# Kernel tuning notes

Hardware: AMD Instinct MI355X
Metric: run time of the kernel (lower is better)

Reference implementation:

```python
import jax, jax.numpy as jnp
import numpy as np

N_NODES = 100000
N_EDGES = 3200000
D_IN = 128


def setup_inputs() -> dict:
    key = jax.random.key(0)
    k1, k2, k3, k4 = jax.random.split(key, 4)
    x = jax.random.normal(k1, (N_NODES, D_IN), dtype=jnp.float32)
    edge_index = jax.random.randint(k2, (2, N_EDGES), 0, N_NODES, dtype=jnp.int64)
    W1 = jax.random.normal(k3, (D_IN, 16), dtype=jnp.float32) * (1.0 / np.sqrt(D_IN))
    b1 = jnp.zeros((16,), dtype=jnp.float32)
    W2 = jax.random.normal(k4, (16, 2), dtype=jnp.float32) * (1.0 / np.sqrt(16))
    b2 = jnp.zeros((2,), dtype=jnp.float32)
    return {"x": x, "edge_index": edge_index, "W1": W1, "b1": b1, "W2": W2, "b2": b2}


def _gcn_norm(edge_index, n_nodes):
    # Add self-loops, then symmetric degree normalization (PyG gcn_norm).
    loops = jnp.arange(n_nodes, dtype=edge_index.dtype)
    row = jnp.concatenate([edge_index[0], loops])  # source
    col = jnp.concatenate([edge_index[1], loops])  # target
    ones = jnp.ones(row.shape[0], dtype=jnp.float32)
    deg = jax.ops.segment_sum(ones, col, num_segments=n_nodes)
    dis = jnp.where(deg > 0, jax.lax.rsqrt(deg), 0.0)  # deg^{-1/2}
    norm = dis[row] * dis[col]  # [E+N]
    return row, col, norm


def _gcn_conv(x, row, col, norm, W, b, n_nodes):
    h = x @ W  # transform first (PyG order): [N, out]
    msgs = h[row] * norm[:, None]  # gather from source, scale
    agg = jax.ops.segment_sum(msgs, col, num_segments=n_nodes)  # scatter-add to target
    return agg + b


def reference(x, edge_index, W1, b1, W2, b2):
    n = x.shape[0]
    row, col, norm = _gcn_norm(edge_index, n)
    h = _gcn_conv(x, row, col, norm, W1, b1, n)
    h = jax.nn.relu(h)
    h = _gcn_conv(h, row, col, norm, W2, b2, n)
    return jax.nn.log_softmax(h, axis=1)
```

## Files before the change

kernel.cpp:

```cpp
#include <hip/hip_runtime.h>
#include <hip/hip_fp16.h>

#define DIN 128
#define BSH 7
#define BSIZE 128
#define NBMAX 800
#define CAP 4480
#define CHUNK 8192
#define PB 512

__global__ __launch_bounds__(PB) void place_kernel(const int* __restrict__ row,
                                                   const int* __restrict__ col,
                                                   int* __restrict__ cur,
                                                   int* __restrict__ sp, int E, int NB) {
    __shared__ int pk[CHUNK];
    __shared__ unsigned short bkid[CHUNK];
    __shared__ int lcnt[NBMAX], lstart[NBMAX], gofs[NBMAX], lcur[NBMAX];
    __shared__ int sst[PB];
    int t = threadIdx.x;
    int e0 = blockIdx.x * CHUNK;
    int cnt = min(CHUNK, E - e0);

    for (int i = t; i < NBMAX; i += PB) { lcnt[i] = 0; lcur[i] = 0; }
    __syncthreads();
    for (int i = t; i < cnt; i += PB)
        atomicAdd(&lcnt[col[e0 + i] >> BSH], 1);
    __syncthreads();
    int b2i = t * 2;
    int v0 = (b2i + 0 < NBMAX) ? lcnt[b2i + 0] : 0;
    int v1 = (b2i + 1 < NBMAX) ? lcnt[b2i + 1] : 0;
    int tot = v0 + v1;
    sst[t] = tot;
    __syncthreads();
    for (int d = 1; d < PB; d <<= 1) {
        int tmp = (t >= d) ? sst[t - d] : 0;
        __syncthreads();
        sst[t] += tmp;
        __syncthreads();
    }
    int ex = sst[t] - tot;
    if (b2i + 0 < NBMAX) lstart[b2i + 0] = ex;
    if (b2i + 1 < NBMAX) lstart[b2i + 1] = ex + v0;
    __syncthreads();
    for (int b = t; b < NB; b += PB) {
        int c = lcnt[b];
        int gb = c ? atomicAdd(&cur[b], c) : 0;
        gofs[b] = b * CAP + gb - lstart[b];
    }
    __syncthreads();
    for (int i = t; i < cnt; i += PB) {
        int r  = row[e0 + i];
        int cc = col[e0 + i];
        int b  = cc >> BSH;
        int rk = atomicAdd(&lcur[b], 1);
        int pos = lstart[b] + rk;
        pk[pos]   = ((cc & (BSIZE - 1)) << 17) | r;
        bkid[pos] = (unsigned short)b;
    }
    __syncthreads();
    for (int i = t; i < cnt; i += PB)
        sp[gofs[bkid[i]] + i] = pk[i];
}

__global__ __launch_bounds__(256) void bdeg_kernel(const int* __restrict__ sp,
                                                   const int* __restrict__ cur,
                                                   float* __restrict__ dis, int N) {
    __shared__ int lcnt[BSIZE];
    int b = blockIdx.x;
    int t = threadIdx.x;
    int cntb = cur[b];
    const int* src = sp + (size_t)b * CAP;
    if (t < BSIZE) lcnt[t] = 0;
    __syncthreads();
    int n4 = cntb >> 2;
    const int4* src4 = (const int4*)src;
    for (int i = t; i < n4; i += 256) {
        int4 v = src4[i];
        atomicAdd(&lcnt[v.x >> 17], 1);
        atomicAdd(&lcnt[v.y >> 17], 1);
        atomicAdd(&lcnt[v.z >> 17], 1);
        atomicAdd(&lcnt[v.w >> 17], 1);
    }
    for (int i = (n4 << 2) + t; i < cntb; i += 256)
        atomicAdd(&lcnt[src[i] >> 17], 1);
    __syncthreads();
    if (t < BSIZE) {
        int gt = b * BSIZE + t;
        if (gt < N) dis[gt] = rsqrtf((float)lcnt[t] + 1.0f);
    }
}

__global__ __launch_bounds__(256) void xw1_kernel(const float* __restrict__ x,
                                                  const float* __restrict__ W1,
                                                  const float* __restrict__ dis,
                                                  __half* __restrict__ hp, int N) {
    __shared__ float xs[64 * 132];
    __shared__ float wt[16 * 132];
    int t = threadIdx.x;
    int base = blockIdx.x * 64;
    for (int i = t; i < DIN * 16; i += 256) {
        int d = i >> 4, k = i & 15;
        wt[k * 132 + d] = W1[i];
    }
    int nrow = min(64, N - base);
    for (int i = t; i < 64 * 32; i += 256) {
        int r = i >> 5, c4 = i & 31;
        float4 v = make_float4(0.f, 0.f, 0.f, 0.f);
        if (r < nrow) v = *(const float4*)(x + (size_t)(base + r) * DIN + c4 * 4);
        *(float4*)(xs + r * 132 + c4 * 4) = v;
    }
    __syncthreads();
    int np = t >> 3;
    int kp = t & 7;
    int n0 = np * 2, k0 = kp * 2;
    const float4* xa = (const float4*)(xs + n0 * 132);
    const float4* xb = (const float4*)(xs + (n0 + 1) * 132);
    const float4* wa = (const float4*)(wt + k0 * 132);
    const float4* wb = (const float4*)(wt + (k0 + 1) * 132);
    float a00 = 0.f, a01 = 0.f, a10 = 0.f, a11 = 0.f;
    #pragma unroll 8
    for (int d4 = 0; d4 < 32; d4++) {
        float4 va = xa[d4], vb = xb[d4], u0 = wa[d4], u1 = wb[d4];
        a00 += va.x*u0.x + va.y*u0.y + va.z*u0.z + va.w*u0.w;
        a01 += va.x*u1.x + va.y*u1.y + va.z*u1.z + va.w*u1.w;
        a10 += vb.x*u0.x + vb.y*u0.y + vb.z*u0.z + vb.w*u0.w;
        a11 += vb.x*u1.x + vb.y*u1.y + vb.z*u1.z + vb.w*u1.w;
    }
    int n = base + n0;
    if (n < N) {
        float d = dis[n];
        hp[(size_t)n * 16 + k0 + 0] = __float2half(a00 * d);
        hp[(size_t)n * 16 + k0 + 1] = __float2half(a01 * d);
    }
    n++;
    if (n < N) {
        float d = dis[n];
        hp[(size_t)n * 16 + k0 + 0] = __float2half(a10 * d);
        hp[(size_t)n * 16 + k0 + 1] = __float2half(a11 * d);
    }
}

__global__ __launch_bounds__(256) void bsg1_kernel(int* sp,
                                                   const int* __restrict__ cur,
                                                   const float* __restrict__ dis,
                                                   const __half2* __restrict__ hp2,
                                                   const float* __restrict__ b1,
                                                   const float* __restrict__ W2,
                                                   int* __restrict__ off,
                                                   float* __restrict__ gp, int N) {
    __shared__ int spk[CAP];
    __shared__ int ss[CAP];
    __shared__ int lcnt[BSIZE], lstart[BSIZE], lcur[BSIZE], sc[BSIZE];
    int b = blockIdx.x;
    int t = threadIdx.x;
    int cntb = cur[b];
    int* reg = sp + (size_t)b * CAP;
    if (t < BSIZE) { lcnt[t] = 0; lcur[t] = 0; }
    __syncthreads();
    for (int i = t; i < cntb; i += 256) {
        int v = reg[i];
        spk[i] = v;
        atomicAdd(&lcnt[v >> 17], 1);
    }
    __syncthreads();
    int v = (t < BSIZE) ? lcnt[t] : 0;
    if (t < BSIZE) sc[t] = v;
    __syncthreads();
    for (int d = 1; d < BSIZE; d <<= 1) {
        int tmp = (t < BSIZE && t >= d) ? sc[t - d] : 0;
        __syncthreads();
        if (t < BSIZE) sc[t] += tmp;
        __syncthreads();
    }
    if (t < BSIZE) lstart[t] = sc[t] - v;
    __syncthreads();
    for (int i = t; i < cntb; i += 256) {
        int vv = spk[i];
        int lt = vv >> 17;
        int rk = atomicAdd(&lcur[lt], 1);
        ss[lstart[lt] + rk] = vv & 0x1FFFF;
    }
    __syncthreads();
    for (int i = t; i < cntb; i += 256) reg[i] = ss[i];
    if (t < BSIZE) {
        off[b * (BSIZE + 1) + t] = b * CAP + lstart[t];
    } else if (t == BSIZE) {
        off[b * (BSIZE + 1) + BSIZE] = b * CAP + cntb;
    }
    int k2  = t & 7;
    int ltg = t >> 3;
    #pragma unroll
    for (int r4 = 0; r4 < 4; r4++) {
        int lt = r4 * 32 + ltg;
        int gt = b * BSIZE + lt;
        if (gt < N) {
            int j0 = lstart[lt];
            int j1 = j0 + lcnt[lt];
            float2 acc0 = __half22float2(hp2[(size_t)gt * 8 + k2]);
            float2 acc1 = make_float2(0.f, 0.f);
            float2 acc2 = make_float2(0.f, 0.f);
            float2 acc3 = make_float2(0.f, 0.f);
            int j = j0;
            for (; j + 3 < j1; j += 4) {
                int r0 = ss[j + 0], r1 = ss[j + 1], r2 = ss[j + 2], r3 = ss[j + 3];
                float2 h0 = __half22float2(hp2[(size_t)r0 * 8 + k2]);
                float2 h1 = __half22float2(hp2[(size_t)r1 * 8 + k2]);
                float2 h2 = __half22float2(hp2[(size_t)r2 * 8 + k2]);
                float2 h3 = __half22float2(hp2[(size_t)r3 * 8 + k2]);
                acc0.x += h0.x; acc0.y += h0.y;
                acc1.x += h1.x; acc1.y += h1.y;
                acc2.x += h2.x; acc2.y += h2.y;
                acc3.x += h3.x; acc3.y += h3.y;
            }
            for (; j < j1; j++) {
                int r = ss[j];
                float2 hv = __half22float2(hp2[(size_t)r * 8 + k2]);
                acc0.x += hv.x; acc0.y += hv.y;
            }
            float2 acc = make_float2(acc0.x + acc1.x + acc2.x + acc3.x,
                                     acc0.y + acc1.y + acc2.y + acc3.y);
            float d = dis[gt];
            int k0 = k2 * 2;
            float v0 = fmaxf(fmaf(acc.x, d, b1[k0 + 0]), 0.0f);
            float v1 = fmaxf(fmaf(acc.y, d, b1[k0 + 1]), 0.0f);
            float p0 = v0 * W2[k0 * 2 + 0] + v1 * W2[k0 * 2 + 2];
            float p1 = v0 * W2[k0 * 2 + 1] + v1 * W2[k0 * 2 + 3];
            p0 += __shfl_xor(p0, 1); p1 += __shfl_xor(p1, 1);
            p0 += __shfl_xor(p0, 2); p1 += __shfl_xor(p1, 2);
            p0 += __shfl_xor(p0, 4); p1 += __shfl_xor(p1, 4);
            if (k2 == 0) *(float2*)(gp + (size_t)gt * 2) = make_float2(p0 * d, p1 * d);
        }
    }
}

__global__ __launch_bounds__(256) void g2_kernel(const int* __restrict__ sp,
                                                 const int* __restrict__ off,
                                                 const float* __restrict__ dis,
                                                 const float* __restrict__ gp,
                                                 const float* __restrict__ b2,
                                                 float* __restrict__ out, int N) {
    int t = blockIdx.x * 256 + threadIdx.x;
    int c    = t >> 2;
    int slot = t & 3;
    if (c >= N) return;
    int idx = (c >> BSH) * (BSIZE + 1) + (c & (BSIZE - 1));
    int j0 = off[idx];
    int j1 = off[idx + 1];
    float a0 = 0.0f, a1v = 0.0f;
    for (int j = j0 + slot; j < j1; j += 4) {
        int r = sp[j];
        float2 gv = *(const float2*)(gp + (size_t)r * 2);
        a0  += gv.x;
        a1v += gv.y;
    }
    a0 += __shfl_xor(a0, 1); a1v += __shfl_xor(a1v, 1);
    a0 += __shfl_xor(a0, 2); a1v += __shfl_xor(a1v, 2);
    if (slot == 0) {
        float2 self = *(const float2*)(gp + (size_t)c * 2);
        float d = dis[c];
        float o0 = (a0  + self.x) * d + b2[0];
        float o1 = (a1v + self.y) * d + b2[1];
        float m = fmaxf(o0, o1);
        float lse = m + logf(expf(o0 - m) + expf(o1 - m));
        *(float2*)(out + (size_t)c * 2) = make_float2(o0 - lse, o1 - lse);
    }
}

extern "C" void kernel_launch(void* const* d_in, const int* in_sizes, int n_in,
                              void* d_out, int out_size, void* d_ws, size_t ws_size,
                              hipStream_t stream) {
    const float* x  = (const float*)d_in[0];
    const int*   ei = (const int*)d_in[1];
    const float* W1 = (const float*)d_in[2];
    const float* b1 = (const float*)d_in[3];
    const float* W2 = (const float*)d_in[4];
    const float* b2 = (const float*)d_in[5];
    float* out = (float*)d_out;

    const int N = in_sizes[0] / DIN;
    const int E = in_sizes[1] / 2;
    const int* row = ei;
    const int* col = ei + E;
    const int NB = (N + BSIZE - 1) / BSIZE;

    int*    cur = (int*)d_ws;
    float*  dis = (float*)(cur + NBMAX);
    int*    off = (int*)(dis + N);
    int*    sp  = off + (size_t)NB * (BSIZE + 1);
    __half* hp  = (__half*)(sp + (size_t)NB * CAP);
    float*  gp  = (float*)(hp + (size_t)N * 16);

    hipMemsetAsync(cur, 0, NBMAX * 4, stream);
    place_kernel<<<(E + CHUNK - 1) / CHUNK, PB, 0, stream>>>(row, col, cur, sp, E, NB);
    bdeg_kernel <<<NB, 256, 0, stream>>>(sp, cur, dis, N);
    xw1_kernel  <<<(N + 63) / 64, 256, 0, stream>>>(x, W1, dis, hp, N);
    bsg1_kernel <<<NB, 256, 0, stream>>>(sp, cur, dis, (const __half2*)hp, b1, W2, off, gp, N);
    g2_kernel   <<<(int)(((size_t)N * 4 + 255) / 256), 256, 0, stream>>>(sp, off, dis, gp, b2, out, N);
}
```

Baseline: 203.4 us.

## Fuse degree computation into xw1 and split bucket sort into half-buckets

Removes the separate degree kernel: each xw1 block scans its parent bucket, counts in-degree for its 64 nodes, writes dis, and applies it from shared memory. The sort-and-gather kernel now runs two blocks per 128-node bucket, each sorting only its half into a new srt2 buffer, which halves shared memory per block and doubles the block count. Each block still reads the whole parent bucket, so bucket reads are duplicated. The second-layer gather uses 8 lanes per node instead of 4.

```diff
diff --git a/kernel.cpp b/kernel.cpp
--- a/kernel.cpp
+++ b/kernel.cpp
@@ -4,8 +4,11 @@
 #define DIN 128
 #define BSH 7
 #define BSIZE 128
+#define HB 64
 #define NBMAX 800
+#define NBMAX2 1600
 #define CAP 4480
+#define HCAP 2560
 #define CHUNK 8192
 #define PB 512
 
@@ -62,42 +65,21 @@
         sp[gofs[bkid[i]] + i] = pk[i];
 }
 
-__global__ __launch_bounds__(256) void bdeg_kernel(const int* __restrict__ sp,
-                                                   const int* __restrict__ cur,
-                                                   float* __restrict__ dis, int N) {
-    __shared__ int lcnt[BSIZE];
-    int b = blockIdx.x;
-    int t = threadIdx.x;
-    int cntb = cur[b];
-    const int* src = sp + (size_t)b * CAP;
-    if (t < BSIZE) lcnt[t] = 0;
-    __syncthreads();
-    int n4 = cntb >> 2;
-    const int4* src4 = (const int4*)src;
-    for (int i = t; i < n4; i += 256) {
-        int4 v = src4[i];
-        atomicAdd(&lcnt[v.x >> 17], 1);
-        atomicAdd(&lcnt[v.y >> 17], 1);
-        atomicAdd(&lcnt[v.z >> 17], 1);
-        atomicAdd(&lcnt[v.w >> 17], 1);
-    }
-    for (int i = (n4 << 2) + t; i < cntb; i += 256)
-        atomicAdd(&lcnt[src[i] >> 17], 1);
-    __syncthreads();
-    if (t < BSIZE) {
-        int gt = b * BSIZE + t;
-        if (gt < N) dis[gt] = rsqrtf((float)lcnt[t] + 1.0f);
-    }
-}
-
 __global__ __launch_bounds__(256) void xw1_kernel(const float* __restrict__ x,
                                                   const float* __restrict__ W1,
-                                                  const float* __restrict__ dis,
+                                                  const int* __restrict__ sp,
+                                                  const int* __restrict__ cur,
+                                                  float* __restrict__ dis,
                                                   __half* __restrict__ hp, int N) {
     __shared__ float xs[64 * 132];
     __shared__ float wt[16 * 132];
+    __shared__ int   lcnt[HB];
+    __shared__ float disl[HB];
     int t = threadIdx.x;
-    int base = blockIdx.x * 64;
+    int blk = blockIdx.x;
+    int base = blk * 64;
+    int B = blk >> 1, h = blk & 1;
+    if (t < HB) lcnt[t] = 0;
     for (int i = t; i < DIN * 16; i += 256) {
         int d = i >> 4, k = i & 15;
         wt[k * 132 + d] = W1[i];
@@ -108,6 +90,20 @@
         float4 v = make_float4(0.f, 0.f, 0.f, 0.f);
         if (r < nrow) v = *(const float4*)(x + (size_t)(base + r) * DIN + c4 * 4);
         *(float4*)(xs + r * 132 + c4 * 4) = v;
+    }
+    __syncthreads();
+    int cntb = cur[B];
+    const int* reg = sp + (size_t)B * CAP;
+    for (int i = t; i < cntb; i += 256) {
+        int lc = reg[i] >> 17;
+        if ((lc >> 6) == h) atomicAdd(&lcnt[lc & 63], 1);
+    }
+    __syncthreads();
+    if (t < HB) {
+        float dv = rsqrtf((float)lcnt[t] + 1.0f);
+        disl[t] = dv;
+        int gt = base + t;
+        if (gt < N) dis[gt] = dv;
     }
     __syncthreads();
     int np = t >> 3;
@@ -128,71 +124,75 @@
     }
     int n = base + n0;
     if (n < N) {
-        float d = dis[n];
+        float d = disl[n0];
         hp[(size_t)n * 16 + k0 + 0] = __float2half(a00 * d);
         hp[(size_t)n * 16 + k0 + 1] = __float2half(a01 * d);
     }
     n++;
     if (n < N) {
-        float d = dis[n];
+        float d = disl[n0 + 1];
         hp[(size_t)n * 16 + k0 + 0] = __float2half(a10 * d);
         hp[(size_t)n * 16 + k0 + 1] = __float2half(a11 * d);
     }
 }
 
-__global__ __launch_bounds__(256) void bsg1_kernel(int* sp,
+__global__ __launch_bounds__(256) void bsg1_kernel(const int* __restrict__ sp,
                                                    const int* __restrict__ cur,
                                                    const float* __restrict__ dis,
                                                    const __half2* __restrict__ hp2,
                                                    const float* __restrict__ b1,
                                                    const float* __restrict__ W2,
+                                                   int* __restrict__ srt2,
                                                    int* __restrict__ off,
                                                    float* __restrict__ gp, int N) {
-    __shared__ int spk[CAP];
-    __shared__ int ss[CAP];
-    __shared__ int lcnt[BSIZE], lstart[BSIZE], lcur[BSIZE], sc[BSIZE];
-    int b = blockIdx.x;
+    __shared__ int ss[HCAP];
+    __shared__ int lcnt[HB], lstart[HB], lcur[HB], sc[HB];
+    int b2 = blockIdx.x;
+    int B = b2 >> 1, h = b2 & 1;
     int t = threadIdx.x;
-    int cntb = cur[b];
-    int* reg = sp + (size_t)b * CAP;
-    if (t < BSIZE) { lcnt[t] = 0; lcur[t] = 0; }
+    int cntb = cur[B];
+    const int* reg = sp + (size_t)B * CAP;
+    if (t < HB) { lcnt[t] = 0; lcur[t] = 0; }
     __syncthreads();
     for (int i = t; i < cntb; i += 256) {
-        int v = reg[i];
-        spk[i] = v;
-        atomicAdd(&lcnt[v >> 17], 1);
-    }
-    __syncthreads();
-    int v = (t < BSIZE) ? lcnt[t] : 0;
-    if (t < BSIZE) sc[t] = v;
-    __syncthreads();
-    for (int d = 1; d < BSIZE; d <<= 1) {
-        int tmp = (t < BSIZE && t >= d) ? sc[t - d] : 0;
+        int lc = reg[i] >> 17;
+        if ((lc >> 6) == h) atomicAdd(&lcnt[lc & 63], 1);
+    }
+    __syncthreads();
+    int v = (t < HB) ? lcnt[t] : 0;
+    if (t < HB) sc[t] = v;
+    __syncthreads();
+    for (int d = 1; d < HB; d <<= 1) {
+        int tmp = (t < HB && t >= d) ? sc[t - d] : 0;
         __syncthreads();
-        if (t < BSIZE) sc[t] += tmp;
+        if (t < HB) sc[t] += tmp;
         __syncthreads();
     }
-    if (t < BSIZE) lstart[t] = sc[t] - v;
+    if (t < HB) lstart[t] = sc[t] - v;
     __syncthreads();
     for (int i = t; i < cntb; i += 256) {
-        int vv = spk[i];
-        int lt = vv >> 17;
-        int rk = atomicAdd(&lcur[lt], 1);
-        ss[lstart[lt] + rk] = vv & 0x1FFFF;
-    }
-    __syncthreads();
-    for (int i = t; i < cntb; i += 256) reg[i] = ss[i];
-    if (t < BSIZE) {
-        off[b * (BSIZE + 1) + t] = b * CAP + lstart[t];
-    } else if (t == BSIZE) {
-        off[b * (BSIZE + 1) + BSIZE] = b * CAP + cntb;
+        int vv = reg[i];
+        int lc = vv >> 17;
+        if ((lc >> 6) == h) {
+            int l = lc & 63;
+            int rk = atomicAdd(&lcur[l], 1);
+            ss[lstart[l] + rk] = vv & 0x1FFFF;
+        }
+    }
+    __syncthreads();
+    int hcnt = sc[HB - 1];
+    for (int i = t; i < hcnt; i += 256) srt2[(size_t)b2 * HCAP + i] = ss[i];
+    if (t < HB) {
+        off[b2 * (HB + 1) + t] = b2 * HCAP + lstart[t];
+    } else if (t == HB) {
+        off[b2 * (HB + 1) + HB] = b2 * HCAP + hcnt;
     }
     int k2  = t & 7;
     int ltg = t >> 3;
     #pragma unroll
-    for (int r4 = 0; r4 < 4; r4++) {
-        int lt = r4 * 32 + ltg;
-        int gt = b * BSIZE + lt;
+    for (int r2 = 0; r2 < 2; r2++) {
+        int lt = r2 * 32 + ltg;
+        int gt = B * BSIZE + h * HB + lt;
         if (gt < N) {
             int j0 = lstart[lt];
             int j1 = j0 + lcnt[lt];
@@ -202,10 +202,10 @@
             float2 acc3 = make_float2(0.f, 0.f);
             int j = j0;
             for (; j + 3 < j1; j += 4) {
-                int r0 = ss[j + 0], r1 = ss[j + 1], r2 = ss[j + 2], r3 = ss[j + 3];
+                int r0 = ss[j + 0], r1 = ss[j + 1], r2i = ss[j + 2], r3 = ss[j + 3];
                 float2 h0 = __half22float2(hp2[(size_t)r0 * 8 + k2]);
                 float2 h1 = __half22float2(hp2[(size_t)r1 * 8 + k2]);
-                float2 h2 = __half22float2(hp2[(size_t)r2 * 8 + k2]);
+                float2 h2 = __half22float2(hp2[(size_t)r2i * 8 + k2]);
                 float2 h3 = __half22float2(hp2[(size_t)r3 * 8 + k2]);
                 acc0.x += h0.x; acc0.y += h0.y;
                 acc1.x += h1.x; acc1.y += h1.y;
@@ -233,28 +233,29 @@
     }
 }
 
-__global__ __launch_bounds__(256) void g2_kernel(const int* __restrict__ sp,
+__global__ __launch_bounds__(256) void g2_kernel(const int* __restrict__ srt2,
                                                  const int* __restrict__ off,
                                                  const float* __restrict__ dis,
                                                  const float* __restrict__ gp,
                                                  const float* __restrict__ b2,
                                                  float* __restrict__ out, int N) {
     int t = blockIdx.x * 256 + threadIdx.x;
-    int c    = t >> 2;
-    int slot = t & 3;
+    int c    = t >> 3;
+    int slot = t & 7;
     if (c >= N) return;
-    int idx = (c >> BSH) * (BSIZE + 1) + (c & (BSIZE - 1));
+    int idx = (c >> 6) * (HB + 1) + (c & 63);
     int j0 = off[idx];
     int j1 = off[idx + 1];
     float a0 = 0.0f, a1v = 0.0f;
-    for (int j = j0 + slot; j < j1; j += 4) {
-        int r = sp[j];
+    for (int j = j0 + slot; j < j1; j += 8) {
+        int r = srt2[j];
         float2 gv = *(const float2*)(gp + (size_t)r * 2);
         a0  += gv.x;
         a1v += gv.y;
     }
     a0 += __shfl_xor(a0, 1); a1v += __shfl_xor(a1v, 1);
     a0 += __shfl_xor(a0, 2); a1v += __shfl_xor(a1v, 2);
+    a0 += __shfl_xor(a0, 4); a1v += __shfl_xor(a1v, 4);
     if (slot == 0) {
         float2 self = *(const float2*)(gp + (size_t)c * 2);
         float d = dis[c];
@@ -281,19 +282,21 @@
     const int E = in_sizes[1] / 2;
     const int* row = ei;
     const int* col = ei + E;
-    const int NB = (N + BSIZE - 1) / BSIZE;
-
-    int*    cur = (int*)d_ws;
-    float*  dis = (float*)(cur + NBMAX);
-    int*    off = (int*)(dis + N);
-    int*    sp  = off + (size_t)NB * (BSIZE + 1);
-    __half* hp  = (__half*)(sp + (size_t)NB * CAP);
-    float*  gp  = (float*)(hp + (size_t)N * 16);
+    const int NB  = (N + BSIZE - 1) / BSIZE;
+    const int NB2 = (N + HB - 1) / HB;
+    const int NG  = NB * 2;
+
+    int*    cur  = (int*)d_ws;
+    float*  dis  = (float*)(cur + NBMAX);
+    int*    off  = (int*)(dis + N);
+    int*    sp   = off + (size_t)NBMAX2 * (HB + 1);
+    int*    srt2 = sp + (size_t)NBMAX * CAP;
+    __half* hp   = (__half*)(srt2 + (size_t)NBMAX2 * HCAP);
+    float*  gp   = (float*)(hp + (size_t)N * 16);
 
     hipMemsetAsync(cur, 0, NBMAX * 4, stream);
     place_kernel<<<(E + CHUNK - 1) / CHUNK, PB, 0, stream>>>(row, col, cur, sp, E, NB);
-    bdeg_kernel <<<NB, 256, 0, stream>>>(sp, cur, dis, N);
-    xw1_kernel  <<<(N + 63) / 64, 256, 0, stream>>>(x, W1, dis, hp, N);
-    bsg1_kernel <<<NB, 256, 0, stream>>>(sp, cur, dis, (const __half2*)hp, b1, W2, off, gp, N);
-    g2_kernel   <<<(int)(((size_t)N * 4 + 255) / 256), 256, 0, stream>>>(sp, off, dis, gp, b2, out, N);
-}
+    xw1_kernel  <<<NB2, 256, 0, stream>>>(x, W1, sp, cur, dis, hp, N);
+    bsg1_kernel <<<NG, 256, 0, stream>>>(sp, cur, dis, (const __half2*)hp, b1, W2, srt2, off, gp, N);
+    g2_kernel   <<<(int)(((size_t)N * 8 + 255) / 256), 256, 0, stream>>>(srt2, off, dis, gp, b2, out, N);
+}
```

Measured after the change: 211.7 us. 4.1% more time.
